# Performance work log

Hardware: AMD Instinct MI355X
Metric: run time of the kernel (lower is better)

## Reference

```python
import jax, jax.numpy as jnp
import numpy as np

NEG_INF = -1e30  # used via -inf literal below; softmax handles -inf fine


def setup_inputs() -> dict:
    key = jax.random.key(0)
    ks = jax.random.split(key, 5)
    B, S, D, O, E = 8, 2048, 1024, 1024, 8
    scale = 1.0 / np.sqrt(D)
    return {
        "x": jax.random.normal(ks[0], (B, S, D), dtype=jnp.float32),
        "gate_w": jax.random.normal(ks[1], (E, D), dtype=jnp.float32) * scale,
        "gate_b": jnp.zeros((E,), dtype=jnp.float32),
        "expert_w": jax.random.normal(ks[2], (E, O, D), dtype=jnp.float32) * scale,
        "expert_b": jnp.zeros((E, O), dtype=jnp.float32),
    }


K = 2  # top-k from module init


def reference(x, gate_w, gate_b, expert_w, expert_b):
    # Gating on sequence-pooled features: [B, D] -> [B, E]
    pooled = x.mean(axis=1)
    logits = pooled @ gate_w.T + gate_b
    topk_vals, _ = jax.lax.top_k(logits, K)
    min_topk = topk_vals[:, -1:]  # k-th largest per row
    masked = jnp.where(logits < min_topk, -jnp.inf, logits)
    gates = jax.nn.softmax(masked, axis=-1)  # [B, E]

    # All experts computed densely: [B, E, S, O]
    expert_out = jax.nn.gelu(
        jnp.einsum('bsd,eod->beso', x, expert_w) + expert_b[None, :, None, :],
        approximate=False,  # torch GELU default is exact erf form
    )
    # Combine with gating weights: [B, S, O]
    return jnp.einsum('be,beso->bso', gates, expert_out)
```

## Files before the change

kernel.cpp:

```cpp
#include <hip/hip_runtime.h>
#include <stdint.h>

constexpr int Bb = 8;
constexpr int Ss = 2048;
constexpr int Dd = 1024;
constexpr int Oo = 1024;
constexpr int Ee = 8;

typedef __bf16 bf16x8 __attribute__((ext_vector_type(8)));
typedef float  f32x4  __attribute__((ext_vector_type(4)));

__device__ __forceinline__ unsigned short f2bf(float f) {
  unsigned int u = __float_as_uint(f);
  unsigned int r = (u + 0x7fffu + ((u >> 16) & 1u)) >> 16;
  return (unsigned short)r;
}

__device__ __forceinline__ void gl_lds16(const void* g, void* l) {
  __builtin_amdgcn_global_load_lds((const __attribute__((address_space(1))) void*)g,
                                   (__attribute__((address_space(3))) void*)l,
                                   16, 0, 0);
}

__global__ __launch_bounds__(256) void k_convert_pool(
    const float* __restrict__ x, unsigned short* __restrict__ xb,
    float* __restrict__ pooled) {
  const int b  = blockIdx.y;
  const int sc = blockIdx.x;
  const int t  = threadIdx.x;
  const size_t base = (size_t)b * Ss * Dd + (size_t)sc * 32 * Dd + t * 4;
  const float4* xp = (const float4*)(x + base);
  ushort4* xo = (ushort4*)(xb + base);
  float4 acc = make_float4(0.f, 0.f, 0.f, 0.f);
#pragma unroll 8
  for (int s = 0; s < 32; ++s) {
    float4 v = xp[(size_t)s * (Dd / 4)];
    acc.x += v.x; acc.y += v.y; acc.z += v.z; acc.w += v.w;
    ushort4 o;
    o.x = f2bf(v.x); o.y = f2bf(v.y); o.z = f2bf(v.z); o.w = f2bf(v.w);
    xo[(size_t)s * (Dd / 4)] = o;
  }
  float* pd = pooled + b * Dd + t * 4;
  atomicAdd(pd + 0, acc.x);
  atomicAdd(pd + 1, acc.y);
  atomicAdd(pd + 2, acc.z);
  atomicAdd(pd + 3, acc.w);
}

__global__ __launch_bounds__(256) void k_convert_w(
    const float* __restrict__ w, unsigned short* __restrict__ wb) {
  size_t i = ((size_t)blockIdx.x * 256 + threadIdx.x) * 4;
  float4 v = *(const float4*)(w + i);
  ushort4 o;
  o.x = f2bf(v.x); o.y = f2bf(v.y); o.z = f2bf(v.z); o.w = f2bf(v.w);
  *(ushort4*)(wb + i) = o;
}

__global__ __launch_bounds__(256) void k_gates(
    const float* __restrict__ pooled, const float* __restrict__ gw,
    const float* __restrict__ gb, int* __restrict__ eidx,
    float* __restrict__ egate) {
  __shared__ float slog[Bb * Ee];
  const int t = threadIdx.x;
  const int p = t >> 2, part = t & 3;
  const int b = p >> 3, e = p & 7;
  const float4* pv = (const float4*)(pooled + b * Dd + part * 256);
  const float4* wv = (const float4*)(gw + e * Dd + part * 256);
  float s = 0.f;
#pragma unroll
  for (int i = 0; i < 64; ++i) {
    float4 a = pv[i], w = wv[i];
    s += a.x * w.x + a.y * w.y + a.z * w.z + a.w * w.w;
  }
  s += __shfl_xor(s, 1);
  s += __shfl_xor(s, 2);
  if (part == 0) slog[p] = s * (1.0f / (float)Ss) + gb[e];
  __syncthreads();
  if (t < Bb) {
    float m1 = -3.4e38f, m2 = -3.4e38f;
    int i1 = 0, i2 = 0;
#pragma unroll
    for (int i = 0; i < Ee; ++i) {
      const float v = slog[t * Ee + i];
      if (v > m1) { m2 = m1; i2 = i1; m1 = v; i1 = i; }
      else if (v > m2) { m2 = v; i2 = i; }
    }
    const float e2 = expf(m2 - m1);
    const float inv = 1.0f / (1.0f + e2);
    eidx[t * 2 + 0] = i1;
    eidx[t * 2 + 1] = i2;
    egate[t * 2 + 0] = inv;
    egate[t * 2 + 1] = e2 * inv;
  }
}

constexpr int BM = 128, BN = 64, BK = 64;
constexpr int STG = 32768;
constexpr int OFF_B0 = 16384, OFF_B1 = 24576;

__global__ __launch_bounds__(256, 2) void k_moe_gemm(
    const unsigned short* __restrict__ xb, const unsigned short* __restrict__ wb,
    const int* __restrict__ eidx, const float* __restrict__ egate,
    const float* __restrict__ expert_b, float* __restrict__ out) {
  __shared__ char lds[2 * STG];

  const int hw = blockIdx.x;
  const int lg_id = ((hw & 7) << 8) | (hw >> 3);
  const int b  = lg_id >> 8;
  const int m0 = (lg_id & 15) * BM;
  const int n0 = ((lg_id >> 4) & 15) * BN;
  const int t  = threadIdx.x;
  const int lane = t & 63;
  const int wid  = t >> 6;
  const int wr = wid >> 1, wc = wid & 1;
  const int lr = lane & 15;
  const int lg = lane >> 4;

  const int e0 = eidx[b * 2 + 0];
  const int e1 = eidx[b * 2 + 1];
  const float g0 = egate[b * 2 + 0];
  const float g1 = egate[b * 2 + 1];

  const int srow = t >> 3;
  const int scol = (((t & 7) ^ (srow & 7)) * 8);
  const int ldsoff = wid * 1024;

  const unsigned short* Abase  = xb + (size_t)b * Ss * Dd + (size_t)m0 * Dd;
  const unsigned short* B0base = wb + (size_t)e0 * Oo * Dd + (size_t)n0 * Dd;
  const unsigned short* B1base = wb + (size_t)e1 * Oo * Dd + (size_t)n0 * Dd;

  f32x4 acc0[4][2] = {};
  f32x4 acc1[4][2] = {};

  auto STAGE = [&](int st, int kt) {
    char* base = lds + st * STG;
#pragma unroll
    for (int h = 0; h < 4; ++h) {
      const int row = srow + h * 32;
      gl_lds16(Abase + (size_t)row * Dd + kt + scol,
               base + h * 4096 + ldsoff);
    }
#pragma unroll
    for (int h = 0; h < 2; ++h) {
      const int row = srow + h * 32;
      const size_t goff = (size_t)row * Dd + kt + scol;
      gl_lds16(B0base + goff, base + OFF_B0 + h * 4096 + ldsoff);
      gl_lds16(B1base + goff, base + OFF_B1 + h * 4096 + ldsoff);
    }
  };

  auto COMPUTE = [&](int st) {
    const char* base = lds + st * STG;
#pragma unroll
    for (int ks = 0; ks < 2; ++ks) {
      const int ul = (ks << 2) | lg;
      bf16x8 af[4], bf0[2], bf1[2];
#pragma unroll
      for (int m = 0; m < 4; ++m) {
        const int r = wr * 64 + m * 16 + lr;
        af[m] = *(const bf16x8*)(base + r * 128 + ((ul ^ (r & 7)) << 4));
      }
#pragma unroll
      for (int n = 0; n < 2; ++n) {
        const int r = wc * 32 + n * 16 + lr;
        bf0[n] = *(const bf16x8*)(base + OFF_B0 + r * 128 + ((ul ^ (r & 7)) << 4));
        bf1[n] = *(const bf16x8*)(base + OFF_B1 + r * 128 + ((ul ^ (r & 7)) << 4));
      }
#pragma unroll
      for (int m = 0; m < 4; ++m)
#pragma unroll
        for (int n = 0; n < 2; ++n) {
          acc0[m][n] = __builtin_amdgcn_mfma_f32_16x16x32_bf16(
              af[m], bf0[n], acc0[m][n], 0, 0, 0);
          acc1[m][n] = __builtin_amdgcn_mfma_f32_16x16x32_bf16(
              af[m], bf1[n], acc1[m][n], 0, 0, 0);
        }
    }
  };

  STAGE(0, 0);
  int cur = 0;
#pragma unroll 1
  for (int kt_i = 0; kt_i < 15; ++kt_i) {
    STAGE(cur ^ 1, (kt_i + 1) * BK);
    asm volatile("s_waitcnt vmcnt(8)" ::: "memory");
    __builtin_amdgcn_s_barrier();
    __builtin_amdgcn_sched_barrier(0);
    COMPUTE(cur);
    __builtin_amdgcn_s_barrier();
    __builtin_amdgcn_sched_barrier(0);
    cur ^= 1;
  }
  asm volatile("s_waitcnt vmcnt(0)" ::: "memory");
  __builtin_amdgcn_s_barrier();
  __builtin_amdgcn_sched_barrier(0);
  COMPUTE(cur);

#pragma unroll
  for (int n = 0; n < 2; ++n) {
    const int col = n0 + wc * 32 + n * 16 + lr;
    const float bias0 = expert_b[e0 * Oo + col];
    const float bias1 = expert_b[e1 * Oo + col];
#pragma unroll
    for (int m = 0; m < 4; ++m)
#pragma unroll
      for (int r = 0; r < 4; ++r) {
        const int row = m0 + wr * 64 + m * 16 + lg * 4 + r;
        const float v0 = acc0[m][n][r] + bias0;
        const float v1 = acc1[m][n][r] + bias1;
        const float ge0 = 0.5f * v0 * (1.0f + erff(v0 * 0.70710678118654752f));
        const float ge1 = 0.5f * v1 * (1.0f + erff(v1 * 0.70710678118654752f));
        out[(size_t)b * Ss * Oo + (size_t)row * Oo + col] = g0 * ge0 + g1 * ge1;
      }
  }
}

extern "C" void kernel_launch(void* const* d_in, const int* in_sizes, int n_in,
                              void* d_out, int out_size, void* d_ws, size_t ws_size,
                              hipStream_t stream) {
  const float* x        = (const float*)d_in[0];
  const float* gate_w   = (const float*)d_in[1];
  const float* gate_b   = (const float*)d_in[2];
  const float* expert_w = (const float*)d_in[3];
  const float* expert_b = (const float*)d_in[4];
  float* out = (float*)d_out;

  char* ws = (char*)d_ws;
  float* pooled = (float*)ws;
  int*   eidx   = (int*)(ws + 32768);
  float* egate  = (float*)(ws + 32768 + 4096);
  unsigned short* xb = (unsigned short*)(ws + 65536);
  unsigned short* wb = (unsigned short*)(ws + 65536 + (size_t)Bb * Ss * Dd * 2);

  hipMemsetAsync(pooled, 0, Bb * Dd * sizeof(float), stream);

  k_convert_pool<<<dim3(64, Bb), 256, 0, stream>>>(x, xb, pooled);
  k_convert_w<<<(Ee * Oo * Dd) / (256 * 4), 256, 0, stream>>>(expert_w, wb);
  k_gates<<<1, 256, 0, stream>>>(pooled, gate_w, gate_b, eidx, egate);
  k_moe_gemm<<<(Ss / BM) * (Oo / BN) * Bb, 256, 0, stream>>>(xb, wb, eidx, egate,
                                                             expert_b, out);
}
```

Before: 274.2 us.

## Fuse prep kernels with last-block gating and streamline GEMM main loop

The x conversion/pooling, weight conversion and gating kernels are merged into a single launch. The gating step runs in whichever block finishes last, detected with an atomic counter and threadfence. This removes two kernel launches and their gaps. The GEMM loop now uses precomputed, incrementing global pointers and LDS offsets, is unrolled by two with constant stage offsets, and raises wave priority around the MFMA bursts to reduce address arithmetic and improve issue. The weight-conversion blocks now loop over 64 chunks each, giving far fewer but longer blocks. The last-block pattern depends on correct memory ordering of the pooled atomics.

```diff
diff --git a/kernel.cpp b/kernel.cpp
--- a/kernel.cpp
+++ b/kernel.cpp
@@ -22,75 +22,90 @@
                                    16, 0, 0);
 }
 
-__global__ __launch_bounds__(256) void k_convert_pool(
+__global__ __launch_bounds__(256) void k_prep(
     const float* __restrict__ x, unsigned short* __restrict__ xb,
-    float* __restrict__ pooled) {
-  const int b  = blockIdx.y;
-  const int sc = blockIdx.x;
-  const int t  = threadIdx.x;
-  const size_t base = (size_t)b * Ss * Dd + (size_t)sc * 32 * Dd + t * 4;
-  const float4* xp = (const float4*)(x + base);
-  ushort4* xo = (ushort4*)(xb + base);
-  float4 acc = make_float4(0.f, 0.f, 0.f, 0.f);
+    const float* __restrict__ w, unsigned short* __restrict__ wb,
+    const float* __restrict__ gw, const float* __restrict__ gb,
+    float* __restrict__ pooled, unsigned int* __restrict__ counter,
+    int* __restrict__ eidx, float* __restrict__ egate) {
+  const int bid = blockIdx.x;
+  const int t = threadIdx.x;
+
+  if (bid >= 512) {
+    const size_t base = (size_t)(bid - 512) * 65536;
+#pragma unroll 4
+    for (int it = 0; it < 64; ++it) {
+      const size_t i = base + (size_t)it * 1024 + t * 4;
+      float4 v = *(const float4*)(w + i);
+      ushort4 o;
+      o.x = f2bf(v.x); o.y = f2bf(v.y); o.z = f2bf(v.z); o.w = f2bf(v.w);
+      *(ushort4*)(wb + i) = o;
+    }
+    return;
+  }
+
+  {
+    const int b  = bid >> 6;
+    const int sc = bid & 63;
+    const size_t base = (size_t)b * Ss * Dd + (size_t)sc * 32 * Dd + t * 4;
+    const float4* xp = (const float4*)(x + base);
+    ushort4* xo = (ushort4*)(xb + base);
+    float4 acc = make_float4(0.f, 0.f, 0.f, 0.f);
 #pragma unroll 8
-  for (int s = 0; s < 32; ++s) {
-    float4 v = xp[(size_t)s * (Dd / 4)];
-    acc.x += v.x; acc.y += v.y; acc.z += v.z; acc.w += v.w;
-    ushort4 o;
-    o.x = f2bf(v.x); o.y = f2bf(v.y); o.z = f2bf(v.z); o.w = f2bf(v.w);
-    xo[(size_t)s * (Dd / 4)] = o;
-  }
-  float* pd = pooled + b * Dd + t * 4;
-  atomicAdd(pd + 0, acc.x);
-  atomicAdd(pd + 1, acc.y);
-  atomicAdd(pd + 2, acc.z);
-  atomicAdd(pd + 3, acc.w);
-}
-
-__global__ __launch_bounds__(256) void k_convert_w(
-    const float* __restrict__ w, unsigned short* __restrict__ wb) {
-  size_t i = ((size_t)blockIdx.x * 256 + threadIdx.x) * 4;
-  float4 v = *(const float4*)(w + i);
-  ushort4 o;
-  o.x = f2bf(v.x); o.y = f2bf(v.y); o.z = f2bf(v.z); o.w = f2bf(v.w);
-  *(ushort4*)(wb + i) = o;
-}
-
-__global__ __launch_bounds__(256) void k_gates(
-    const float* __restrict__ pooled, const float* __restrict__ gw,
-    const float* __restrict__ gb, int* __restrict__ eidx,
-    float* __restrict__ egate) {
-  __shared__ float slog[Bb * Ee];
-  const int t = threadIdx.x;
-  const int p = t >> 2, part = t & 3;
-  const int b = p >> 3, e = p & 7;
-  const float4* pv = (const float4*)(pooled + b * Dd + part * 256);
-  const float4* wv = (const float4*)(gw + e * Dd + part * 256);
-  float s = 0.f;
-#pragma unroll
-  for (int i = 0; i < 64; ++i) {
-    float4 a = pv[i], w = wv[i];
-    s += a.x * w.x + a.y * w.y + a.z * w.z + a.w * w.w;
-  }
-  s += __shfl_xor(s, 1);
-  s += __shfl_xor(s, 2);
-  if (part == 0) slog[p] = s * (1.0f / (float)Ss) + gb[e];
+    for (int s = 0; s < 32; ++s) {
+      float4 v = xp[(size_t)s * (Dd / 4)];
+      acc.x += v.x; acc.y += v.y; acc.z += v.z; acc.w += v.w;
+      ushort4 o;
+      o.x = f2bf(v.x); o.y = f2bf(v.y); o.z = f2bf(v.z); o.w = f2bf(v.w);
+      xo[(size_t)s * (Dd / 4)] = o;
+    }
+    float* pd = pooled + b * Dd + t * 4;
+    atomicAdd(pd + 0, acc.x);
+    atomicAdd(pd + 1, acc.y);
+    atomicAdd(pd + 2, acc.z);
+    atomicAdd(pd + 3, acc.w);
+  }
+
+  __shared__ unsigned s_last;
+  __threadfence();
+  if (t == 0) {
+    unsigned v = atomicAdd(counter, 1u);
+    s_last = (v == 511u) ? 1u : 0u;
+  }
   __syncthreads();
-  if (t < Bb) {
-    float m1 = -3.4e38f, m2 = -3.4e38f;
-    int i1 = 0, i2 = 0;
-#pragma unroll
-    for (int i = 0; i < Ee; ++i) {
-      const float v = slog[t * Ee + i];
-      if (v > m1) { m2 = m1; i2 = i1; m1 = v; i1 = i; }
-      else if (v > m2) { m2 = v; i2 = i; }
-    }
-    const float e2 = expf(m2 - m1);
-    const float inv = 1.0f / (1.0f + e2);
-    eidx[t * 2 + 0] = i1;
-    eidx[t * 2 + 1] = i2;
-    egate[t * 2 + 0] = inv;
-    egate[t * 2 + 1] = e2 * inv;
+  if (s_last) {
+    __threadfence();
+    __shared__ float slog[Bb * Ee];
+    const int p = t >> 2, part = t & 3;
+    const int b = p >> 3, e = p & 7;
+    const float4* pv = (const float4*)(pooled + b * Dd + part * 256);
+    const float4* wv = (const float4*)(gw + e * Dd + part * 256);
+    float s = 0.f;
+#pragma unroll
+    for (int i = 0; i < 64; ++i) {
+      float4 a = pv[i], wq = wv[i];
+      s += a.x * wq.x + a.y * wq.y + a.z * wq.z + a.w * wq.w;
+    }
+    s += __shfl_xor(s, 1);
+    s += __shfl_xor(s, 2);
+    if (part == 0) slog[p] = s * (1.0f / (float)Ss) + gb[e];
+    __syncthreads();
+    if (t < Bb) {
+      float m1 = -3.4e38f, m2 = -3.4e38f;
+      int i1 = 0, i2 = 0;
+#pragma unroll
+      for (int i = 0; i < Ee; ++i) {
+        const float v = slog[t * Ee + i];
+        if (v > m1) { m2 = m1; i2 = i1; m1 = v; i1 = i; }
+        else if (v > m2) { m2 = v; i2 = i; }
+      }
+      const float e2 = expf(m2 - m1);
+      const float inv = 1.0f / (1.0f + e2);
+      eidx[t * 2 + 0] = i1;
+      eidx[t * 2 + 1] = i2;
+      egate[t * 2 + 0] = inv;
+      egate[t * 2 + 1] = e2 * inv;
+    }
   }
 }
 
@@ -125,76 +140,107 @@
   const int scol = (((t & 7) ^ (srow & 7)) * 8);
   const int ldsoff = wid * 1024;
 
-  const unsigned short* Abase  = xb + (size_t)b * Ss * Dd + (size_t)m0 * Dd;
-  const unsigned short* B0base = wb + (size_t)e0 * Oo * Dd + (size_t)n0 * Dd;
-  const unsigned short* B1base = wb + (size_t)e1 * Oo * Dd + (size_t)n0 * Dd;
+  const unsigned short* gA[4];
+  const unsigned short* gB0[2];
+  const unsigned short* gB1[2];
+  {
+    const unsigned short* Abase  = xb + (size_t)b * Ss * Dd + (size_t)m0 * Dd;
+    const unsigned short* B0base = wb + (size_t)e0 * Oo * Dd + (size_t)n0 * Dd;
+    const unsigned short* B1base = wb + (size_t)e1 * Oo * Dd + (size_t)n0 * Dd;
+#pragma unroll
+    for (int h = 0; h < 4; ++h) gA[h] = Abase + (size_t)(srow + h * 32) * Dd + scol;
+#pragma unroll
+    for (int h = 0; h < 2; ++h) {
+      gB0[h] = B0base + (size_t)(srow + h * 32) * Dd + scol;
+      gB1[h] = B1base + (size_t)(srow + h * 32) * Dd + scol;
+    }
+  }
+
+  int offA[2][4], offB[2][2];
+#pragma unroll
+  for (int ks = 0; ks < 2; ++ks) {
+    const int ul = (ks << 2) | lg;
+#pragma unroll
+    for (int m = 0; m < 4; ++m) {
+      const int r = wr * 64 + m * 16 + lr;
+      offA[ks][m] = r * 128 + ((ul ^ (r & 7)) << 4);
+    }
+#pragma unroll
+    for (int n = 0; n < 2; ++n) {
+      const int r = wc * 32 + n * 16 + lr;
+      offB[ks][n] = OFF_B0 + r * 128 + ((ul ^ (r & 7)) << 4);
+    }
+  }
 
   f32x4 acc0[4][2] = {};
   f32x4 acc1[4][2] = {};
 
-  auto STAGE = [&](int st, int kt) {
-    char* base = lds + st * STG;
+  auto STAGE = [&](char* base) {
 #pragma unroll
     for (int h = 0; h < 4; ++h) {
-      const int row = srow + h * 32;
-      gl_lds16(Abase + (size_t)row * Dd + kt + scol,
-               base + h * 4096 + ldsoff);
+      gl_lds16(gA[h], base + h * 4096 + ldsoff);
+      gA[h] += BK;
     }
 #pragma unroll
     for (int h = 0; h < 2; ++h) {
-      const int row = srow + h * 32;
-      const size_t goff = (size_t)row * Dd + kt + scol;
-      gl_lds16(B0base + goff, base + OFF_B0 + h * 4096 + ldsoff);
-      gl_lds16(B1base + goff, base + OFF_B1 + h * 4096 + ldsoff);
+      gl_lds16(gB0[h], base + OFF_B0 + h * 4096 + ldsoff);
+      gl_lds16(gB1[h], base + OFF_B1 + h * 4096 + ldsoff);
+      gB0[h] += BK;
+      gB1[h] += BK;
     }
   };
 
-  auto COMPUTE = [&](int st) {
-    const char* base = lds + st * STG;
-#pragma unroll
-    for (int ks = 0; ks < 2; ++ks) {
-      const int ul = (ks << 2) | lg;
-      bf16x8 af[4], bf0[2], bf1[2];
-#pragma unroll
-      for (int m = 0; m < 4; ++m) {
-        const int r = wr * 64 + m * 16 + lr;
-        af[m] = *(const bf16x8*)(base + r * 128 + ((ul ^ (r & 7)) << 4));
-      }
-#pragma unroll
-      for (int n = 0; n < 2; ++n) {
-        const int r = wc * 32 + n * 16 + lr;
-        bf0[n] = *(const bf16x8*)(base + OFF_B0 + r * 128 + ((ul ^ (r & 7)) << 4));
-        bf1[n] = *(const bf16x8*)(base + OFF_B1 + r * 128 + ((ul ^ (r & 7)) << 4));
-      }
-#pragma unroll
-      for (int m = 0; m < 4; ++m)
-#pragma unroll
-        for (int n = 0; n < 2; ++n) {
-          acc0[m][n] = __builtin_amdgcn_mfma_f32_16x16x32_bf16(
-              af[m], bf0[n], acc0[m][n], 0, 0, 0);
-          acc1[m][n] = __builtin_amdgcn_mfma_f32_16x16x32_bf16(
-              af[m], bf1[n], acc1[m][n], 0, 0, 0);
-        }
-    }
-  };
-
-  STAGE(0, 0);
-  int cur = 0;
+#define COMPUTE_STEP(STOFF)                                                   \
+  {                                                                           \
+    _Pragma("unroll")                                                         \
+    for (int ks = 0; ks < 2; ++ks) {                                          \
+      bf16x8 af[4], bf0[2], bf1[2];                                           \
+      _Pragma("unroll")                                                       \
+      for (int m = 0; m < 4; ++m)                                             \
+        af[m] = *(const bf16x8*)(lds + offA[ks][m] + (STOFF));                \
+      _Pragma("unroll")                                                       \
+      for (int n = 0; n < 2; ++n) {                                           \
+        bf0[n] = *(const bf16x8*)(lds + offB[ks][n] + (STOFF));               \
+        bf1[n] = *(const bf16x8*)(lds + offB[ks][n] + 8192 + (STOFF));        \
+      }                                                                       \
+      __builtin_amdgcn_s_setprio(1);                                          \
+      _Pragma("unroll")                                                       \
+      for (int m = 0; m < 4; ++m) {                                           \
+        _Pragma("unroll")                                                     \
+        for (int n = 0; n < 2; ++n) {                                         \
+          acc0[m][n] = __builtin_amdgcn_mfma_f32_16x16x32_bf16(               \
+              af[m], bf0[n], acc0[m][n], 0, 0, 0);                            \
+          acc1[m][n] = __builtin_amdgcn_mfma_f32_16x16x32_bf16(               \
+              af[m], bf1[n], acc1[m][n], 0, 0, 0);                            \
+        }                                                                     \
+      }                                                                       \
+      __builtin_amdgcn_s_setprio(0);                                         \
+    }                                                                         \
+  }
+
+#define PHASE(STAGE_BASE, STOFF)                                              \
+  STAGE(STAGE_BASE);                                                          \
+  asm volatile("s_waitcnt vmcnt(8)" ::: "memory");                            \
+  __builtin_amdgcn_s_barrier();                                               \
+  __builtin_amdgcn_sched_barrier(0);                                          \
+  COMPUTE_STEP(STOFF);                                                        \
+  __builtin_amdgcn_s_barrier();                                               \
+  __builtin_amdgcn_sched_barrier(0);
+
+  STAGE(lds);
 #pragma unroll 1
-  for (int kt_i = 0; kt_i < 15; ++kt_i) {
-    STAGE(cur ^ 1, (kt_i + 1) * BK);
-    asm volatile("s_waitcnt vmcnt(8)" ::: "memory");
-    __builtin_amdgcn_s_barrier();
-    __builtin_amdgcn_sched_barrier(0);
-    COMPUTE(cur);
-    __builtin_amdgcn_s_barrier();
-    __builtin_amdgcn_sched_barrier(0);
-    cur ^= 1;
-  }
+  for (int i = 0; i < 7; ++i) {
+    PHASE(lds + STG, 0);
+    PHASE(lds, STG);
+  }
+  PHASE(lds + STG, 0);
   asm volatile("s_waitcnt vmcnt(0)" ::: "memory");
   __builtin_amdgcn_s_barrier();
   __builtin_amdgcn_sched_barrier(0);
-  COMPUTE(cur);
+  COMPUTE_STEP(STG);
+
+#undef PHASE
+#undef COMPUTE_STEP
 
 #pragma unroll
   for (int n = 0; n < 2; ++n) {
@@ -227,16 +273,16 @@
 
   char* ws = (char*)d_ws;
   float* pooled = (float*)ws;
-  int*   eidx   = (int*)(ws + 32768);
-  float* egate  = (float*)(ws + 32768 + 4096);
+  unsigned int* counter = (unsigned int*)(ws + 32768);
+  int*   eidx   = (int*)(ws + 32832);
+  float* egate  = (float*)(ws + 32896);
   unsigned short* xb = (unsigned short*)(ws + 65536);
   unsigned short* wb = (unsigned short*)(ws + 65536 + (size_t)Bb * Ss * Dd * 2);
 
-  hipMemsetAsync(pooled, 0, Bb * Dd * sizeof(float), stream);
-
-  k_convert_pool<<<dim3(64, Bb), 256, 0, stream>>>(x, xb, pooled);
-  k_convert_w<<<(Ee * Oo * Dd) / (256 * 4), 256, 0, stream>>>(expert_w, wb);
-  k_gates<<<1, 256, 0, stream>>>(pooled, gate_w, gate_b, eidx, egate);
+  hipMemsetAsync(ws, 0, 32772, stream);
+
+  k_prep<<<640, 256, 0, stream>>>(x, xb, expert_w, wb, gate_w, gate_b,
+                                  pooled, counter, eidx, egate);
   k_moe_gemm<<<(Ss / BM) * (Oo / BN) * Bb, 256, 0, stream>>>(xb, wb, eidx, egate,
                                                              expert_b, out);
 }
```

After: 374.4 us. +36.5%, slower.
